# Kernel tuning notes

Hardware: AMD Instinct MI355X
Metric: run time of the kernel (lower is better)

Reference implementation:

```python
import jax, jax.numpy as jnp
import numpy as np

NEG_INF = -1e12  # matches masked_fill value -1000000000000.0
LEAKY_SLOPE = 0.2


def setup_inputs() -> dict:
    key = jax.random.key(0)
    k1, k2, k3, k4, k5 = jax.random.split(key, 5)
    B, C, H, N, F_IN, F_OUT = 4, 4, 4, 1024, 64, 64
    h = jax.random.normal(k1, (B, C, N, F_IN), dtype=jnp.float32)
    adj = jax.random.randint(k2, (B, N, N), 0, 2).astype(jnp.float32)
    w = jax.random.normal(k3, (C, H, F_IN, F_OUT), dtype=jnp.float32) * 0.1
    a_src = jax.random.normal(k4, (C, H, F_OUT, 1), dtype=jnp.float32) * 0.1
    a_dst = jax.random.normal(k5, (C, H, F_OUT, 1), dtype=jnp.float32) * 0.1
    return {"h": h, "adj": adj, "w": w, "a_src": a_src, "a_dst": a_dst}


def reference(h, adj, w, a_src, a_dst):
    # h: [B,C,N,f_in], w: [C,H,f_in,f_out] -> h_prime: [B,C,H,N,f_out]
    h_prime = jnp.einsum('bcnf,chfo->bchno', h, w)
    t = jnp.tanh(h_prime)
    # additive attention scores: [B,C,H,N]
    attn_src = jnp.einsum('bchno,cho->bchn', t, a_src[..., 0])
    attn_dst = jnp.einsum('bchno,cho->bchn', t, a_dst[..., 0])
    # attn[b,c,h,i,j] = src[i] + dst[j]  -> [B,C,H,N,N]
    attn = attn_src[..., :, None] + attn_dst[..., None, :]
    attn = jnp.where(attn >= 0, attn, LEAKY_SLOPE * attn)  # leaky_relu(0.2)
    N = h.shape[2]
    adj_sl = adj + jnp.eye(N, dtype=adj.dtype)  # add self-loops
    mask = (adj_sl == 0)[:, None, None, :, :]   # [B,1,1,N,N]
    attn = jnp.where(mask, NEG_INF, attn)
    attn = jax.nn.softmax(attn, axis=-1)
    # dropout is identity (attn_dropout=0.0 / eval mode)
    out = jnp.einsum('bchnm,bchmo->bchno', attn, h_prime)
    return out
```

## Files before the change

### kernel.cpp

```cpp
#include <hip/hip_runtime.h>
#include <hip/hip_bf16.h>
#include <math.h>

#define NB 4
#define NC 4
#define NH 4
#define NN 1024
#define NF 64
#define NCOMBO 64
#define LEAK 0.2f

typedef __attribute__((ext_vector_type(8)))  short  short8;
typedef __attribute__((ext_vector_type(16))) float  float16;

static __device__ __forceinline__ unsigned pk_bf16(float a, float b) {
    union { __hip_bfloat162 h; unsigned u; } cv;
    cv.h = __float22bfloat162_rn(make_float2(a, b));
    return cv.u;
}

static __device__ __forceinline__ float fast_tanh(float x) {
    const float e = __expf(2.f * x);
    return 1.f - 2.f * __builtin_amdgcn_rcpf(1.f + e);
}

static __device__ __forceinline__ void async_cp16(const void* gsrc, void* ldst) {
    __builtin_amdgcn_global_load_lds(
        (const __attribute__((address_space(1))) unsigned int*)gsrc,
        (__attribute__((address_space(3))) unsigned int*)ldst, 16, 0, 0);
}

static __device__ __forceinline__ void split8(const float4 a, const float4 b,
                                              short8* hi, short8* lo) {
    union { short8 v; unsigned u[4]; } H, L;
    const float x[8] = {a.x,a.y,a.z,a.w,b.x,b.y,b.z,b.w};
    float lov[8];
    #pragma unroll
    for (int p = 0; p < 4; ++p) {
        const unsigned pk = pk_bf16(x[2*p], x[2*p+1]);
        H.u[p] = pk;
        union { unsigned u; float f; } f0, f1;
        f0.u = pk << 16; f1.u = pk & 0xffff0000u;
        lov[2*p]   = x[2*p]   - f0.f;
        lov[2*p+1] = x[2*p+1] - f1.f;
    }
    #pragma unroll
    for (int p = 0; p < 4; ++p) L.u[p] = pk_bf16(lov[2*p], lov[2*p+1]);
    *hi = H.v; *lo = L.v;
}

__global__ __launch_bounds__(256) void gA_produce(
    const float* __restrict__ h, const float* __restrict__ adj,
    const float* __restrict__ w, const float* __restrict__ a_src,
    const float* __restrict__ a_dst,
    unsigned short* __restrict__ hpt, float* __restrict__ asrc,
    float* __restrict__ edPt, float* __restrict__ edNt,
    unsigned long long* __restrict__ bits)
{
    __shared__ __align__(16) char smem[17920];
    float* w_s    = (float*)smem;
    unsigned short* whi = (unsigned short*)smem;
    unsigned short* wlo = (unsigned short*)(smem + 8192);
    float* as_lds = (float*)(smem + 16384);
    float* ad_lds = (float*)(smem + 16640);
    float* scS    = (float*)(smem + 16896);
    float* scD    = (float*)(smem + 17408);

    const int idx  = blockIdx.x;
    const int t    = threadIdx.x;
    const int g    = (idx & 7)*8 + ((idx >> 3) & 7);
    const int tile = idx >> 6;
    const int b = g >> 4, c = (g >> 2) & 3, hh = g & 3;
    const int lane = t & 63, l31 = lane & 31, half = lane >> 5;
    const int wv = t >> 6, rg = wv >> 1, oh = wv & 1;

    const float4* wsrc = (const float4*)(w + ((size_t)(c*NH + hh))*NF*NF);
    #pragma unroll
    for (int i = 0; i < 4; ++i)
        ((float4*)w_s)[t + i*256] = wsrc[t + i*256];
    if (t < NF) {
        as_lds[t] = a_src[(c*NH + hh)*NF + t];
        ad_lds[t] = a_dst[(c*NH + hh)*NF + t];
    }
    __syncthreads();

    float wv0[8], wv1[8];
    {
        const int n = t & 31;
        #pragma unroll
        for (int j = 0; j < 8; ++j) {
            const int blk0 = t >> 5, blk1 = (t >> 5) + 8;
            const int k0 = (blk0 >> 2)*16 + (blk0 & 1)*8 + j;
            const int o0 = ((blk0 >> 1) & 1)*32 + n;
            const int k1 = (blk1 >> 2)*16 + (blk1 & 1)*8 + j;
            const int o1 = ((blk1 >> 1) & 1)*32 + n;
            wv0[j] = w_s[k0*64 + o0];
            wv1[j] = w_s[k1*64 + o1];
        }
    }
    short8 ahi[4], alo[4];
    {
        const float* hrow = h +
            (((size_t)(b*NC + c))*NN + tile*64 + rg*32 + l31)*NF;
        #pragma unroll
        for (int s = 0; s < 4; ++s) {
            const float4 v0 = *(const float4*)&hrow[s*16 + half*8];
            const float4 v1 = *(const float4*)&hrow[s*16 + half*8 + 4];
            split8(v0, v1, &ahi[s], &alo[s]);
        }
    }
    __syncthreads();

    {
        union { short8 v; unsigned u[4]; } H; short8 L;
        float4 a0 = make_float4(wv0[0],wv0[1],wv0[2],wv0[3]);
        float4 a1 = make_float4(wv0[4],wv0[5],wv0[6],wv0[7]);
        split8(a0, a1, &H.v, &L);
        *(short8*)&whi[((t >> 5)*32 + (t & 31))*8] = H.v;
        *(short8*)&wlo[((t >> 5)*32 + (t & 31))*8] = L;
        a0 = make_float4(wv1[0],wv1[1],wv1[2],wv1[3]);
        a1 = make_float4(wv1[4],wv1[5],wv1[6],wv1[7]);
        split8(a0, a1, &H.v, &L);
        *(short8*)&whi[(((t >> 5) + 8)*32 + (t & 31))*8] = H.v;
        *(short8*)&wlo[(((t >> 5) + 8)*32 + (t & 31))*8] = L;
    }
    __syncthreads();

    float16 acc;
    #pragma unroll
    for (int i = 0; i < 16; ++i) acc[i] = 0.f;
    #pragma unroll
    for (int s = 0; s < 4; ++s) {
        const short8 bhi = *(const short8*)&whi[(((s*2 + oh)*2 + half)*32 + l31)*8];
        const short8 blo = *(const short8*)&wlo[(((s*2 + oh)*2 + half)*32 + l31)*8];
        acc = __builtin_amdgcn_mfma_f32_32x32x16_bf16(ahi[s], bhi, acc, 0, 0, 0);
        acc = __builtin_amdgcn_mfma_f32_32x32x16_bf16(alo[s], bhi, acc, 0, 0, 0);
        acc = __builtin_amdgcn_mfma_f32_32x32x16_bf16(ahi[s], blo, acc, 0, 0, 0);
    }

    {
        const int col = oh*32 + l31;
        const float av = as_lds[col], dv = ad_lds[col];
        float sS[16], sD[16];
        #pragma unroll
        for (int reg = 0; reg < 16; ++reg) {
            const float tt = fast_tanh(acc[reg]);
            sS[reg] = tt * av;
            sD[reg] = tt * dv;
        }
        #pragma unroll
        for (int off = 1; off <= 16; off <<= 1) {
            #pragma unroll
            for (int reg = 0; reg < 16; ++reg) {
                sS[reg] += __shfl_xor(sS[reg], off);
                sD[reg] += __shfl_xor(sD[reg], off);
            }
        }
        if (l31 == 0) {
            #pragma unroll
            for (int reg = 0; reg < 16; ++reg) {
                const int row = rg*32 + (reg & 3) + 8*(reg >> 2) + 4*half;
                scS[row*2 + oh] = sS[reg];
                scD[row*2 + oh] = sD[reg];
            }
        }
    }

    {
        unsigned short* dst = hpt + ((size_t)(g*16 + tile))*4096;
        #pragma unroll
        for (int q = 0; q < 4; ++q) {
            const int ks = rg*2 + (q >> 1), hf = q & 1;
            const int elem = (((ks*2 + oh)*2 + hf)*32 + l31)*8 + 4*half;
            uint2 pk;
            pk.x = pk_bf16(acc[q*4 + 0], acc[q*4 + 1]);
            pk.y = pk_bf16(acc[q*4 + 2], acc[q*4 + 3]);
            *(uint2*)&dst[elem] = pk;
        }
    }
    __syncthreads();
    if (t < 64) {
        const float s = scS[t*2] + scS[t*2 + 1];
        const float d = scD[t*2] + scD[t*2 + 1];
        asrc[(size_t)g*NN + tile*64 + t] = s;
        edPt[(size_t)g*NN + tile*64 + t] = __expf(d);
        edNt[(size_t)g*NN + tile*64 + t] = __expf(LEAK*d);
    }

    {
        const int base = idx*4096;
        #pragma unroll
        for (int q = 0; q < 16; ++q) {
            const int e  = base + q*256 + t;
            const int j  = e & (NN-1);
            const int i  = (e >> 10) & (NN-1);
            const int bb = e >> 20;
            const bool pred = (adj[e] != 0.f) || (j == i);
            const unsigned long long m = __ballot(pred);
            if ((t & 63) == 0) bits[((size_t)bb*NN + i)*16 + (j >> 6)] = m;
        }
    }
}

__global__ __launch_bounds__(256, 4) void gC_attn(
    const unsigned short* __restrict__ hpt, const float* __restrict__ asrc,
    const float* __restrict__ edPt, const float* __restrict__ edNt,
    const unsigned long long* __restrict__ bits, float* __restrict__ out)
{
    __shared__ __align__(16) char smem[29696];
    unsigned short* fragB = (unsigned short*)smem;
    unsigned*       tbl   = (unsigned*)(smem + 16384);
    float*          comb  = (float*)smem;
    unsigned long long* bits_lds = (unsigned long long*)(smem + 20480);
    float*          psum2 = (float*)(smem + 29184);

    const int idx = blockIdx.x;
    const int t   = threadIdx.x;
    const int g   = (idx & 7)*8 + ((idx >> 3) & 7);
    const int it  = idx >> 6;
    const int b   = g >> 4;
    const int i0  = it*64;
    const int wv = t >> 6, lane = t & 63;
    const int l31 = lane & 31, half = lane >> 5;
    const int rg = wv >> 1, jh = wv & 1;
    const int myrow = rg*32 + l31;

    {
        const char* gs = (const char*)hpt + ((size_t)g*16)*8192 + wv*2048 + lane*16;
        char* ls = smem + wv*2048;
        async_cp16(gs, ls);
        async_cp16(gs + 1024, ls + 1024);
    }
    #pragma unroll
    for (int q = 0; q < 4; ++q) {
        const int j = q*256 + t;
        tbl[j] = pk_bf16(edNt[(size_t)g*NN + j], edPt[(size_t)g*NN + j]);
    }
    {
        const unsigned long long* bsrc = bits + ((size_t)b*NN + i0)*16;
        #pragma unroll
        for (int q = 0; q < 4; ++q) {
            const int e = q*256 + t;
            bits_lds[(e >> 4)*17 + (e & 15)] = bsrc[e];
        }
    }
    const float sv    = asrc[(size_t)g*NN + i0 + myrow];
    const float ratio = __expf((LEAK - 1.f)*sv);

    union { short8 v; unsigned short u[8]; } ONES;
    #pragma unroll
    for (int i = 0; i < 8; ++i) ONES.u[i] = 0x3F80;

    float16 acc0, acc1, acc2;
    #pragma unroll
    for (int i = 0; i < 16; ++i) { acc0[i] = 0.f; acc1[i] = 0.f; acc2[i] = 0.f; }

    for (int jt = 0; jt < 16; ++jt) {
        __syncthreads();
        const int fb = jt & 1;
        if (jt < 15) {
            const char* gs = (const char*)hpt + ((size_t)g*16 + jt + 1)*8192
                             + wv*2048 + lane*16;
            char* ls = smem + ((jt + 1) & 1)*8192 + wv*2048;
            async_cp16(gs, ls);
            async_cp16(gs + 1024, ls + 1024);
        }
        const unsigned long long wb = bits_lds[myrow*17 + jt];

        #pragma unroll
        for (int kk = 0; kk < 2; ++kk) {
            const int ks = jh*2 + kk;
            const int jo = ks*16 + half*8;
            const uint4 Ta = *(const uint4*)&tbl[jt*64 + jo];
            const uint4 Tb = *(const uint4*)&tbl[jt*64 + jo + 4];
            const short8 b0 = *(const short8*)
                &fragB[fb*4096 + (((ks*2 + 0)*2 + half)*32 + l31)*8];
            const short8 b1 = *(const short8*)
                &fragB[fb*4096 + (((ks*2 + 1)*2 + half)*32 + l31)*8];
            const unsigned bb = (unsigned)(wb >> jo) & 0xffu;

            float p0, p1, p2, p3, p4, p5, p6, p7;
            {
                union { unsigned u; float f; } hi, lo;
                hi.u = Ta.x & 0xffff0000u; lo.u = Ta.x << 16;
                p0 = fmaxf(hi.f, ratio*lo.f); p0 = (bb & 1u)   ? p0 : 0.f;
                hi.u = Ta.y & 0xffff0000u; lo.u = Ta.y << 16;
                p1 = fmaxf(hi.f, ratio*lo.f); p1 = (bb & 2u)   ? p1 : 0.f;
                hi.u = Ta.z & 0xffff0000u; lo.u = Ta.z << 16;
                p2 = fmaxf(hi.f, ratio*lo.f); p2 = (bb & 4u)   ? p2 : 0.f;
                hi.u = Ta.w & 0xffff0000u; lo.u = Ta.w << 16;
                p3 = fmaxf(hi.f, ratio*lo.f); p3 = (bb & 8u)   ? p3 : 0.f;
                hi.u = Tb.x & 0xffff0000u; lo.u = Tb.x << 16;
                p4 = fmaxf(hi.f, ratio*lo.f); p4 = (bb & 16u)  ? p4 : 0.f;
                hi.u = Tb.y & 0xffff0000u; lo.u = Tb.y << 16;
                p5 = fmaxf(hi.f, ratio*lo.f); p5 = (bb & 32u)  ? p5 : 0.f;
                hi.u = Tb.z & 0xffff0000u; lo.u = Tb.z << 16;
                p6 = fmaxf(hi.f, ratio*lo.f); p6 = (bb & 64u)  ? p6 : 0.f;
                hi.u = Tb.w & 0xffff0000u; lo.u = Tb.w << 16;
                p7 = fmaxf(hi.f, ratio*lo.f); p7 = (bb & 128u) ? p7 : 0.f;
            }

            union { short8 v; unsigned u[4]; } af;
            af.u[0] = pk_bf16(p0, p1);
            af.u[1] = pk_bf16(p2, p3);
            af.u[2] = pk_bf16(p4, p5);
            af.u[3] = pk_bf16(p6, p7);

            acc2 = __builtin_amdgcn_mfma_f32_32x32x16_bf16(af.v, ONES.v, acc2, 0, 0, 0);
            acc0 = __builtin_amdgcn_mfma_f32_32x32x16_bf16(af.v, b0,     acc0, 0, 0, 0);
            acc1 = __builtin_amdgcn_mfma_f32_32x32x16_bf16(af.v, b1,     acc1, 0, 0, 0);
        }
    }

    __syncthreads();

    if (l31 == 0) {
        #pragma unroll
        for (int reg = 0; reg < 16; ++reg) {
            const int r = (reg & 3) + 8*(reg >> 2) + 4*half;
            psum2[jh*64 + rg*32 + r] = acc2[reg];
        }
    }
    if (jh == 1) {
        float* cb = comb + (rg*64 + lane)*34;
        #pragma unroll
        for (int i = 0; i < 8; ++i) {
            float2 v0; v0.x = acc0[2*i]; v0.y = acc0[2*i+1];
            float2 v1; v1.x = acc1[2*i]; v1.y = acc1[2*i+1];
            *(float2*)&cb[2*i]      = v0;
            *(float2*)&cb[16 + 2*i] = v1;
        }
    }
    __syncthreads();
    if (jh == 0) {
        const float* cb = comb + (rg*64 + lane)*34;
        #pragma unroll
        for (int i = 0; i < 8; ++i) {
            const float2 v0 = *(const float2*)&cb[2*i];
            const float2 v1 = *(const float2*)&cb[16 + 2*i];
            acc0[2*i] += v0.x; acc0[2*i+1] += v0.y;
            acc1[2*i] += v1.x; acc1[2*i+1] += v1.y;
        }
        #pragma unroll
        for (int reg = 0; reg < 16; ++reg) {
            const int r = (reg & 3) + 8*(reg >> 2) + 4*half;
            const int row = rg*32 + r;
            const float inv = __builtin_amdgcn_rcpf(psum2[row] + psum2[64 + row]);
            const size_t base = ((size_t)g*NN + i0 + row)*NF;
            out[base + l31]      = acc0[reg] * inv;
            out[base + l31 + 32] = acc1[reg] * inv;
        }
    }
}

extern "C" void kernel_launch(void* const* d_in, const int* in_sizes, int n_in,
                              void* d_out, int out_size, void* d_ws, size_t ws_size,
                              hipStream_t stream)
{
    const float* h     = (const float*)d_in[0];
    const float* adj   = (const float*)d_in[1];
    const float* w     = (const float*)d_in[2];
    const float* a_src = (const float*)d_in[3];
    const float* a_dst = (const float*)d_in[4];
    float* out = (float*)d_out;

    char* ws = (char*)d_ws;
    unsigned short* hpt = (unsigned short*)ws;
    float* asrc         = (float*)(ws + 8388608);
    float* edP          = (float*)(ws + 8388608 + 262144);
    float* edN          = (float*)(ws + 8388608 + 524288);
    unsigned long long* bits = (unsigned long long*)(ws + 8388608 + 786432);

    gA_produce<<<dim3(1024), dim3(256), 0, stream>>>(
        h, adj, w, a_src, a_dst, hpt, asrc, edP, edN, bits);
    gC_attn<<<dim3(1024), dim3(256), 0, stream>>>(
        hpt, asrc, edP, edN, bits, out);
}
```

Before: 118.9 us.

## Load B fragments directly from global with register prefetch, drop LDS double-buffer

The attention kernel no longer stages h_prime B-fragments through a double-buffered LDS ring filled by async global-to-LDS copies. Each lane now loads its fragments straight from global memory into registers, prefetching one step ahead, and the loop becomes fully unrolled with no per-tile barriers. The exp tables are kept as separate fp32 arrays instead of a packed bf16 pair, and masking uses a bit-extract AND instead of selects. This removes 16 __syncthreads and shrinks LDS, which could allow more resident blocks. In exchange, the kernel relies on global or cache latency being hidden by a single-step prefetch, does more LDS reads per step for the fp32 tables, and raises register pressure from the full unroll.

After: 115.5 us. 1.03x faster.

```diff
diff --git a/kernel.cpp b/kernel.cpp
--- a/kernel.cpp
+++ b/kernel.cpp
@@ -24,10 +24,15 @@
     return 1.f - 2.f * __builtin_amdgcn_rcpf(1.f + e);
 }
 
-static __device__ __forceinline__ void async_cp16(const void* gsrc, void* ldst) {
-    __builtin_amdgcn_global_load_lds(
-        (const __attribute__((address_space(1))) unsigned int*)gsrc,
-        (__attribute__((address_space(3))) unsigned int*)ldst, 16, 0, 0);
+static __device__ __forceinline__ float mask_by_bit(float p, unsigned bb, int k) {
+#if defined(__has_builtin) && __has_builtin(__builtin_amdgcn_sbfe)
+    const int m = __builtin_amdgcn_sbfe((int)bb, k, 1);
+#else
+    const int m = -(int)((bb >> k) & 1u);
+#endif
+    union { float f; int i; } u;
+    u.f = p; u.i &= m;
+    return u.f;
 }
 
 static __device__ __forceinline__ void split8(const float4 a, const float4 b,
@@ -207,12 +212,12 @@
     const float* __restrict__ edPt, const float* __restrict__ edNt,
     const unsigned long long* __restrict__ bits, float* __restrict__ out)
 {
-    __shared__ __align__(16) char smem[29696];
-    unsigned short* fragB = (unsigned short*)smem;
-    unsigned*       tbl   = (unsigned*)(smem + 16384);
-    float*          comb  = (float*)smem;
-    unsigned long long* bits_lds = (unsigned long long*)(smem + 20480);
-    float*          psum2 = (float*)(smem + 29184);
+    __shared__ __align__(16) char smem[17920];
+    float* edP_lds = (float*)smem;
+    float* edN_lds = (float*)(smem + 4096);
+    unsigned long long* bits_lds = (unsigned long long*)(smem + 8192);
+    float* comb  = (float*)smem;
+    float* psum2 = (float*)(smem + 17408);
 
     const int idx = blockIdx.x;
     const int t   = threadIdx.x;
@@ -225,16 +230,11 @@
     const int rg = wv >> 1, jh = wv & 1;
     const int myrow = rg*32 + l31;
 
-    {
-        const char* gs = (const char*)hpt + ((size_t)g*16)*8192 + wv*2048 + lane*16;
-        char* ls = smem + wv*2048;
-        async_cp16(gs, ls);
-        async_cp16(gs + 1024, ls + 1024);
-    }
     #pragma unroll
     for (int q = 0; q < 4; ++q) {
         const int j = q*256 + t;
-        tbl[j] = pk_bf16(edNt[(size_t)g*NN + j], edPt[(size_t)g*NN + j]);
+        edP_lds[j] = edPt[(size_t)g*NN + j];
+        edN_lds[j] = edNt[(size_t)g*NN + j];
     }
     {
         const unsigned long long* bsrc = bits + ((size_t)b*NN + i0)*16;
@@ -246,6 +246,7 @@
     }
     const float sv    = asrc[(size_t)g*NN + i0 + myrow];
     const float ratio = __expf((LEAK - 1.f)*sv);
+    __syncthreads();
 
     union { short8 v; unsigned short u[8]; } ONES;
     #pragma unroll
@@ -255,61 +256,56 @@
     #pragma unroll
     for (int i = 0; i < 16; ++i) { acc0[i] = 0.f; acc1[i] = 0.f; acc2[i] = 0.f; }
 
-    for (int jt = 0; jt < 16; ++jt) {
-        __syncthreads();
-        const int fb = jt & 1;
-        if (jt < 15) {
-            const char* gs = (const char*)hpt + ((size_t)g*16 + jt + 1)*8192
-                             + wv*2048 + lane*16;
-            char* ls = smem + ((jt + 1) & 1)*8192 + wv*2048;
-            async_cp16(gs, ls);
-            async_cp16(gs + 1024, ls + 1024);
-        }
+    const unsigned short* hb = hpt + (size_t)g*16*4096;
+
+    short8 b0, b1;
+    {
+        const int ks = jh*2;
+        b0 = *(const short8*)&hb[(((ks*2 + 0)*2 + half)*32 + l31)*8];
+        b1 = *(const short8*)&hb[(((ks*2 + 1)*2 + half)*32 + l31)*8];
+    }
+
+    #pragma unroll
+    for (int m = 0; m < 32; ++m) {
+        const int jt = m >> 1, kk = m & 1;
+        const int ks = jh*2 + kk;
+        const int jo = ks*16 + half*8;
+
+        short8 nb0, nb1;
+        if (m < 31) {
+            const int jt1 = (m + 1) >> 1, kk1 = (m + 1) & 1;
+            const int ks1 = jh*2 + kk1;
+            const size_t base1 = (size_t)jt1*4096;
+            nb0 = *(const short8*)&hb[base1 + (((ks1*2 + 0)*2 + half)*32 + l31)*8];
+            nb1 = *(const short8*)&hb[base1 + (((ks1*2 + 1)*2 + half)*32 + l31)*8];
+        }
+
         const unsigned long long wb = bits_lds[myrow*17 + jt];
-
-        #pragma unroll
-        for (int kk = 0; kk < 2; ++kk) {
-            const int ks = jh*2 + kk;
-            const int jo = ks*16 + half*8;
-            const uint4 Ta = *(const uint4*)&tbl[jt*64 + jo];
-            const uint4 Tb = *(const uint4*)&tbl[jt*64 + jo + 4];
-            const short8 b0 = *(const short8*)
-                &fragB[fb*4096 + (((ks*2 + 0)*2 + half)*32 + l31)*8];
-            const short8 b1 = *(const short8*)
-                &fragB[fb*4096 + (((ks*2 + 1)*2 + half)*32 + l31)*8];
-            const unsigned bb = (unsigned)(wb >> jo) & 0xffu;
-
-            float p0, p1, p2, p3, p4, p5, p6, p7;
-            {
-                union { unsigned u; float f; } hi, lo;
-                hi.u = Ta.x & 0xffff0000u; lo.u = Ta.x << 16;
-                p0 = fmaxf(hi.f, ratio*lo.f); p0 = (bb & 1u)   ? p0 : 0.f;
-                hi.u = Ta.y & 0xffff0000u; lo.u = Ta.y << 16;
-                p1 = fmaxf(hi.f, ratio*lo.f); p1 = (bb & 2u)   ? p1 : 0.f;
-                hi.u = Ta.z & 0xffff0000u; lo.u = Ta.z << 16;
-                p2 = fmaxf(hi.f, ratio*lo.f); p2 = (bb & 4u)   ? p2 : 0.f;
-                hi.u = Ta.w & 0xffff0000u; lo.u = Ta.w << 16;
-                p3 = fmaxf(hi.f, ratio*lo.f); p3 = (bb & 8u)   ? p3 : 0.f;
-                hi.u = Tb.x & 0xffff0000u; lo.u = Tb.x << 16;
-                p4 = fmaxf(hi.f, ratio*lo.f); p4 = (bb & 16u)  ? p4 : 0.f;
-                hi.u = Tb.y & 0xffff0000u; lo.u = Tb.y << 16;
-                p5 = fmaxf(hi.f, ratio*lo.f); p5 = (bb & 32u)  ? p5 : 0.f;
-                hi.u = Tb.z & 0xffff0000u; lo.u = Tb.z << 16;
-                p6 = fmaxf(hi.f, ratio*lo.f); p6 = (bb & 64u)  ? p6 : 0.f;
-                hi.u = Tb.w & 0xffff0000u; lo.u = Tb.w << 16;
-                p7 = fmaxf(hi.f, ratio*lo.f); p7 = (bb & 128u) ? p7 : 0.f;
-            }
-
-            union { short8 v; unsigned u[4]; } af;
-            af.u[0] = pk_bf16(p0, p1);
-            af.u[1] = pk_bf16(p2, p3);
-            af.u[2] = pk_bf16(p4, p5);
-            af.u[3] = pk_bf16(p6, p7);
-
-            acc2 = __builtin_amdgcn_mfma_f32_32x32x16_bf16(af.v, ONES.v, acc2, 0, 0, 0);
-            acc0 = __builtin_amdgcn_mfma_f32_32x32x16_bf16(af.v, b0,     acc0, 0, 0, 0);
-            acc1 = __builtin_amdgcn_mfma_f32_32x32x16_bf16(af.v, b1,     acc1, 0, 0, 0);
-        }
+        const unsigned bb = (unsigned)(wb >> jo) & 0xffu;
+
+        const float4 P0 = *(const float4*)&edP_lds[jt*64 + jo];
+        const float4 P1 = *(const float4*)&edP_lds[jt*64 + jo + 4];
+        const float4 Q0 = *(const float4*)&edN_lds[jt*64 + jo];
+        const float4 Q1 = *(const float4*)&edN_lds[jt*64 + jo + 4];
+        const float Pp[8] = {P0.x,P0.y,P0.z,P0.w,P1.x,P1.y,P1.z,P1.w};
+        const float Nv[8] = {Q0.x,Q0.y,Q0.z,Q0.w,Q1.x,Q1.y,Q1.z,Q1.w};
+
+        float pv[8];
+        #pragma unroll
+        for (int e2 = 0; e2 < 8; ++e2)
+            pv[e2] = mask_by_bit(fmaxf(Pp[e2], ratio*Nv[e2]), bb, e2);
+
+        union { short8 v; unsigned u[4]; } af;
+        af.u[0] = pk_bf16(pv[0], pv[1]);
+        af.u[1] = pk_bf16(pv[2], pv[3]);
+        af.u[2] = pk_bf16(pv[4], pv[5]);
+        af.u[3] = pk_bf16(pv[6], pv[7]);
+
+        acc2 = __builtin_amdgcn_mfma_f32_32x32x16_bf16(af.v, ONES.v, acc2, 0, 0, 0);
+        acc0 = __builtin_amdgcn_mfma_f32_32x32x16_bf16(af.v, b0,     acc0, 0, 0, 0);
+        acc1 = __builtin_amdgcn_mfma_f32_32x32x16_bf16(af.v, b1,     acc1, 0, 0, 0);
+
+        if (m < 31) { b0 = nb0; b1 = nb1; }
     }
 
     __syncthreads();
```
